# Kernel optimization log

Hardware: AMD Instinct MI355X
Metric: run time of the kernel (lower is better)

Reference implementation:

```python
import jax, jax.numpy as jnp
import numpy as np


def setup_inputs() -> dict:
    key = jax.random.key(0)
    k1, k2, k3 = jax.random.split(key, 3)
    B, S, D, H = 16, 4096, 512, 512
    inp = jax.random.normal(k1, (B, S, D), dtype=jnp.float32)
    # torch nn.Linear(D, 3*H): weight (3H, D), bias (3H,)
    W = jax.random.normal(k2, (3 * H, D), dtype=jnp.float32) * (1.0 / np.sqrt(D))
    b = jax.random.normal(k3, (3 * H,), dtype=jnp.float32) * 0.01
    return {"inp": inp, "W": W, "b": b}


def _forget_mult(z, f):
    # z, f: (B, S, H). h_t = f_t*z_t + (1-f_t)*h_{t-1}, h_{-1}=0 (hid=None)
    zt = jnp.swapaxes(z, 0, 1)  # (S, B, H)
    ft = jnp.swapaxes(f, 0, 1)
    h0 = jnp.zeros(z.shape[0:1] + z.shape[2:3], dtype=z.dtype)  # (B, H)

    def step(h, zf):
        zi, fi = zf
        h = fi * zi + (1.0 - fi) * h
        return h, h

    _, hs = jax.lax.scan(step, h0, (zt, ft))
    return jnp.swapaxes(hs, 0, 1)  # (B, S, H)


def reference(inp, W, b):
    # QRNNLayer forward: window=1, output_gate=True, batch_first=True,
    # backward=False, zoneout=0, hid=None.
    y = jnp.einsum('bsd,hd->bsh', inp, W) + b  # (B, S, 3H)
    z_gate, f_gate, o_gate = jnp.split(y, 3, axis=2)
    z_gate = jnp.tanh(z_gate)
    f_gate = jax.nn.sigmoid(f_gate)
    c_gate = _forget_mult(z_gate, f_gate)
    output = jax.nn.sigmoid(o_gate) * c_gate
    return output, c_gate[:, -1]
```

## Files before the change

kernel.cpp:

```cpp
#include <hip/hip_runtime.h>
#include <stdint.h>

#define Bdim 16
#define Sdim 4096
#define Hdim 512
#define Mdim (Bdim*Sdim)
#define N3   (3*Hdim)
#define Kdim 512
#define NCHUNK 64
#define CLEN  (Sdim/NCHUNK)

typedef __bf16 bf16;
typedef __bf16 bf16x4 __attribute__((ext_vector_type(4)));
typedef __bf16 bf16x8 __attribute__((ext_vector_type(8)));
typedef float  f32x4  __attribute__((ext_vector_type(4)));
typedef _Float16 f16;
typedef _Float16 f16x4 __attribute__((ext_vector_type(4)));
typedef _Float16 f16x8 __attribute__((ext_vector_type(8)));

__device__ __forceinline__ void gload_lds16(const void* g, void* l) {
  __builtin_amdgcn_global_load_lds(
      (const __attribute__((address_space(1))) uint32_t*)g,
      (__attribute__((address_space(3))) uint32_t*)l, 16, 0, 0);
}

__global__ void __launch_bounds__(256) cvt_kernel(const float4* __restrict__ in,
                                                  bf16x4* __restrict__ out, int n4) {
  int i = blockIdx.x * blockDim.x + threadIdx.x;
  if (i >= n4) return;
  float4 v = in[i];
  bf16x4 o;
  o.x = (bf16)v.x; o.y = (bf16)v.y; o.z = (bf16)v.z; o.w = (bf16)v.w;
  out[i] = o;
}

#define BM 256
#define BN 256
#define BK2 32
#define NT (Kdim/BK2)

__global__ void __launch_bounds__(512, 2) gemm_act_kernel(
    const bf16* __restrict__ A, const bf16* __restrict__ Wb,
    const float* __restrict__ bias,
    f16* __restrict__ zbuf, f16* __restrict__ fbuf, f16* __restrict__ ogbuf) {
  __shared__ char lds[65536];
  const int tid  = threadIdx.x;
  const int wid  = tid >> 6;
  const int lane = tid & 63;
  const int wr = wid >> 2, wc = wid & 3;
  const int bid = blockIdx.x;
  const int wg  = (bid & 7) * 192 + (bid >> 3);
  const int mt = wg / (N3 / BN);
  const int nt = wg % (N3 / BN);
  const int row0 = mt * BM;

  const bf16* Ag = A  + (size_t)row0 * Kdim;
  const bf16* Bg = Wb + (size_t)(nt * BN) * Kdim;

  uint32_t srcO[2];
  {
    int r_ = tid >> 2, slot = tid & 3;
    #pragma unroll
    for (int i = 0; i < 2; ++i) {
      int row = i * 128 + r_;
      srcO[i] = (uint32_t)(row * Kdim + ((slot ^ ((row >> 1) & 3)) << 3));
    }
  }
  const uint32_t dstBase = (uint32_t)(wid * 1024);

  uint32_t byteA[8], byteB[4];
  {
    int kslot = lane >> 4;
    #pragma unroll
    for (int m = 0; m < 8; ++m) {
      int row = wr * 128 + m * 16 + (lane & 15);
      byteA[m] = (uint32_t)(row * 64 + ((kslot ^ ((row >> 1) & 3)) << 4));
    }
    #pragma unroll
    for (int n = 0; n < 4; ++n) {
      int row = wc * 64 + n * 16 + (lane & 15);
      byteB[n] = (uint32_t)(16384 + row * 64 + ((kslot ^ ((row >> 1) & 3)) << 4));
    }
  }

  f32x4 acc[8][4];
  #pragma unroll
  for (int m = 0; m < 8; ++m)
    #pragma unroll
    for (int n = 0; n < 4; ++n)
      acc[m][n] = (f32x4){0.f, 0.f, 0.f, 0.f};

  {
    char* Ad = lds; char* Bd = lds + 16384;
    #pragma unroll
    for (int i = 0; i < 2; ++i) gload_lds16(Ag + srcO[i], Ad + i * 8192 + dstBase);
    #pragma unroll
    for (int i = 0; i < 2; ++i) gload_lds16(Bg + srcO[i], Bd + i * 8192 + dstBase);
  }
  __syncthreads();

  for (int t = 0; t < NT; ++t) {
    if (t + 1 < NT) {
      char* Ad = lds + ((t + 1) & 1) * 32768; char* Bd = Ad + 16384;
      #pragma unroll
      for (int i = 0; i < 2; ++i)
        gload_lds16(Ag + srcO[i] + (t + 1) * BK2, Ad + i * 8192 + dstBase);
      #pragma unroll
      for (int i = 0; i < 2; ++i)
        gload_lds16(Bg + srcO[i] + (t + 1) * BK2, Bd + i * 8192 + dstBase);
    }
    const char* Ab = lds + (t & 1) * 32768;
    bf16x8 af[8], bfrag[4];
    #pragma unroll
    for (int m = 0; m < 8; ++m) af[m] = *(const bf16x8*)(Ab + byteA[m]);
    #pragma unroll
    for (int n = 0; n < 4; ++n) bfrag[n] = *(const bf16x8*)(Ab + byteB[n]);
    __builtin_amdgcn_s_setprio(1);
    #pragma unroll
    for (int m = 0; m < 8; ++m)
      #pragma unroll
      for (int n = 0; n < 4; ++n)
        acc[m][n] = __builtin_amdgcn_mfma_f32_16x16x32_bf16(af[m], bfrag[n], acc[m][n], 0, 0, 0);
    __builtin_amdgcn_s_setprio(0);
    __syncthreads();
  }

  const int gate = nt >> 1;
  const int cbn  = (nt & 1) * 256;
  f16* dst = (gate == 0) ? zbuf : ((gate == 1) ? fbuf : ogbuf);
  float bv[4];
  #pragma unroll
  for (int n = 0; n < 4; ++n)
    bv[n] = bias[gate * Hdim + cbn + wc * 64 + n * 16 + (lane & 15)];

  #pragma unroll
  for (int R = 0; R < 2; ++R) {
    #pragma unroll
    for (int m4 = 0; m4 < 4; ++m4) {
      const int m = R * 4 + m4;
      #pragma unroll
      for (int n = 0; n < 4; ++n) {
        int col = wc * 64 + n * 16 + (lane & 15);
        #pragma unroll
        for (int r = 0; r < 4; ++r) {
          int Lrow = wr * 64 + m4 * 16 + (lane >> 4) * 4 + r;
          float y = acc[m][n][r] + bv[n];
          float v;
          if (gate == 0) {
            float e = __expf(2.f * y);
            v = 1.f - 2.f / (e + 1.f);
          } else {
            v = 1.f / (1.f + __expf(-y));
          }
          uint32_t byte = (uint32_t)(Lrow * 512 + col * 2) ^ ((uint32_t)(Lrow & 7) << 4);
          *(f16*)(lds + byte) = (f16)v;
        }
      }
    }
    __syncthreads();
    #pragma unroll
    for (int j = 0; j < 8; ++j) {
      int c = j * 512 + tid;
      int Lrow = c >> 5, col8 = c & 31;
      uint32_t byte = (uint32_t)(Lrow * 512 + col8 * 16) ^ ((uint32_t)(Lrow & 7) << 4);
      f16x8 v = *(const f16x8*)(lds + byte);
      int G = (Lrow >> 6) * 128 + R * 64 + (Lrow & 63);
      *(f16x8*)&dst[(size_t)(row0 + G) * Hdim + cbn + col8 * 8] = v;
    }
    __syncthreads();
  }
}

__global__ void __launch_bounds__(256) scanA_kernel(const f16x4* __restrict__ z4,
                                                    const f16x4* __restrict__ f4,
                                                    float* __restrict__ Pb,
                                                    float* __restrict__ Qb) {
  int u  = blockIdx.x * blockDim.x + threadIdx.x;
  int hq = u & 127;
  int bc = u >> 7;
  int b  = bc & (Bdim - 1);
  int c  = bc >> 4;
  size_t base = ((size_t)(b * Sdim + c * CLEN)) * 128 + hq;
  float P[4] = {1.f, 1.f, 1.f, 1.f}, Q[4] = {0.f, 0.f, 0.f, 0.f};
  #pragma unroll 4
  for (int s = 0; s < CLEN; ++s) {
    f16x4 fv = f4[base], zv = z4[base];
    #pragma unroll
    for (int j = 0; j < 4; ++j) {
      float f = (float)fv[j];
      Q[j] += f * ((float)zv[j] - Q[j]);
      P[j] *= (1.f - f);
    }
    base += 128;
  }
  int outi = ((c * Bdim + b) << 9) + hq * 4;
  *(float4*)&Pb[outi] = make_float4(P[0], P[1], P[2], P[3]);
  *(float4*)&Qb[outi] = make_float4(Q[0], Q[1], Q[2], Q[3]);
}

__global__ void __launch_bounds__(256) scanB_kernel(const float* __restrict__ Pb,
                                                    const float* __restrict__ Qb,
                                                    float* __restrict__ hin,
                                                    float* __restrict__ c_last) {
  int t = blockIdx.x * blockDim.x + threadIdx.x;
  int h = t & (Hdim - 1), b = t >> 9;
  float hs = 0.f;
  #pragma unroll 8
  for (int c = 0; c < NCHUNK; ++c) {
    hin[c * (Bdim * Hdim) + t] = hs;
    int u = ((c * Bdim + b) << 9) + h;
    hs = Pb[u] * hs + Qb[u];
  }
  c_last[t] = hs;
}

__global__ void __launch_bounds__(256) scanC_kernel(const f16x4* __restrict__ z4,
                                                    const f16x4* __restrict__ f4,
                                                    const f16x4* __restrict__ og4,
                                                    const float* __restrict__ hin,
                                                    float4* __restrict__ out4) {
  int u  = blockIdx.x * blockDim.x + threadIdx.x;
  int hq = u & 127;
  int bc = u >> 7;
  int b  = bc & (Bdim - 1);
  int c  = bc >> 4;
  float4 hv = *(const float4*)&hin[c * (Bdim * Hdim) + b * Hdim + hq * 4];
  float h[4] = {hv.x, hv.y, hv.z, hv.w};
  size_t base = ((size_t)(b * Sdim + c * CLEN)) * 128 + hq;
  #pragma unroll 4
  for (int s = 0; s < CLEN; ++s) {
    f16x4 fv = f4[base], zv = z4[base], ov = og4[base];
    float4 o;
    #pragma unroll
    for (int j = 0; j < 4; ++j) {
      h[j] += (float)fv[j] * ((float)zv[j] - h[j]);
    }
    o.x = (float)ov[0] * h[0]; o.y = (float)ov[1] * h[1];
    o.z = (float)ov[2] * h[2]; o.w = (float)ov[3] * h[3];
    out4[base] = o;
    base += 128;
  }
}

extern "C" void kernel_launch(void* const* d_in, const int* in_sizes, int n_in,
                              void* d_out, int out_size, void* d_ws, size_t ws_size,
                              hipStream_t stream) {
  const float* inp  = (const float*)d_in[0];
  const float* W    = (const float*)d_in[1];
  const float* bias = (const float*)d_in[2];
  float* out = (float*)d_out;

  char* ws = (char*)d_ws;
  bf16* Abf = (bf16*)(ws);
  bf16* Wbf = (bf16*)(ws + 67108864);
  f16*  zh  = (f16*) (ws + 68681728);
  f16*  fh  = (f16*) (ws + 135790592);
  f16*  ogh = (f16*) (ws + 202899456);
  float* Pb = (float*)(ws + 270008320);
  float* Qb = (float*)(ws + 272105472);
  float* hin= (float*)(ws + 274202624);

  {
    int n4 = (Mdim * Kdim) / 4;
    cvt_kernel<<<n4 / 256, 256, 0, stream>>>((const float4*)inp, (bf16x4*)Abf, n4);
  }
  {
    int n4 = (N3 * Kdim) / 4;
    cvt_kernel<<<n4 / 256, 256, 0, stream>>>((const float4*)W, (bf16x4*)Wbf, n4);
  }
  gemm_act_kernel<<<(Mdim / BM) * (N3 / BN), 512, 0, stream>>>(Abf, Wbf, bias,
                                                               zh, fh, ogh);
  scanA_kernel<<<(NCHUNK * Bdim * 128) / 256, 256, 0, stream>>>(
      (const f16x4*)zh, (const f16x4*)fh, Pb, Qb);
  scanB_kernel<<<(Bdim * Hdim) / 256, 256, 0, stream>>>(Pb, Qb, hin,
                                                        out + (size_t)Mdim * Hdim);
  scanC_kernel<<<(NCHUNK * Bdim * 128) / 256, 256, 0, stream>>>(
      (const f16x4*)zh, (const f16x4*)fh, (const f16x4*)ogh, hin, (float4*)out);
}
```

Baseline: 313.9 us.

## Shrink GEMM tile to 128 rows, fuse conversions, widen scan vectors, double chunks

The GEMM M-tile drops from 256 to 128 rows with smaller LDS buffers and launch bounds of 4 waves per SIMD. This aims at higher occupancy and more workgroups, at the cost of less A/B reuse per tile and the removal of the setprio hints. The two fp32→bf16 conversion launches are merged into one kernel. The scan kernels now process 8 halves per thread and the number of scan chunks doubles to 128, which gives more parallelism but adds more carry work in scanB.

```diff
diff --git a/kernel.cpp b/kernel.cpp
--- a/kernel.cpp
+++ b/kernel.cpp
@@ -7,7 +7,7 @@
 #define Mdim (Bdim*Sdim)
 #define N3   (3*Hdim)
 #define Kdim 512
-#define NCHUNK 64
+#define NCHUNK 128
 #define CLEN  (Sdim/NCHUNK)
 
 typedef __bf16 bf16;
@@ -15,7 +15,6 @@
 typedef __bf16 bf16x8 __attribute__((ext_vector_type(8)));
 typedef float  f32x4  __attribute__((ext_vector_type(4)));
 typedef _Float16 f16;
-typedef _Float16 f16x4 __attribute__((ext_vector_type(4)));
 typedef _Float16 f16x8 __attribute__((ext_vector_type(8)));
 
 __device__ __forceinline__ void gload_lds16(const void* g, void* l) {
@@ -24,32 +23,37 @@
       (__attribute__((address_space(3))) uint32_t*)l, 16, 0, 0);
 }
 
-__global__ void __launch_bounds__(256) cvt_kernel(const float4* __restrict__ in,
-                                                  bf16x4* __restrict__ out, int n4) {
+__global__ void __launch_bounds__(256) cvt2_kernel(const float4* __restrict__ a,
+                                                   bf16x4* __restrict__ oa, int nA,
+                                                   const float4* __restrict__ w,
+                                                   bf16x4* __restrict__ ow, int nW) {
   int i = blockIdx.x * blockDim.x + threadIdx.x;
-  if (i >= n4) return;
-  float4 v = in[i];
+  const float4* src; bf16x4* dst; int j;
+  if (i < nA) { src = a; dst = oa; j = i; }
+  else { j = i - nA; if (j >= nW) return; src = w; dst = ow; }
+  float4 v = src[j];
   bf16x4 o;
   o.x = (bf16)v.x; o.y = (bf16)v.y; o.z = (bf16)v.z; o.w = (bf16)v.w;
-  out[i] = o;
-}
-
-#define BM 256
+  dst[j] = o;
+}
+
+#define BM 128
 #define BN 256
 #define BK2 32
 #define NT (Kdim/BK2)
-
-__global__ void __launch_bounds__(512, 2) gemm_act_kernel(
+#define LBUF 24576
+
+__global__ void __launch_bounds__(512, 4) gemm_act_kernel(
     const bf16* __restrict__ A, const bf16* __restrict__ Wb,
     const float* __restrict__ bias,
     f16* __restrict__ zbuf, f16* __restrict__ fbuf, f16* __restrict__ ogbuf) {
-  __shared__ char lds[65536];
+  __shared__ char lds[2 * LBUF];
   const int tid  = threadIdx.x;
   const int wid  = tid >> 6;
   const int lane = tid & 63;
   const int wr = wid >> 2, wc = wid & 3;
   const int bid = blockIdx.x;
-  const int wg  = (bid & 7) * 192 + (bid >> 3);
+  const int wg  = (bid & 7) * 384 + (bid >> 3);
   const int mt = wg / (N3 / BN);
   const int nt = wg % (N3 / BN);
   const int row0 = mt * BM;
@@ -57,71 +61,69 @@
   const bf16* Ag = A  + (size_t)row0 * Kdim;
   const bf16* Bg = Wb + (size_t)(nt * BN) * Kdim;
 
-  uint32_t srcO[2];
-  {
-    int r_ = tid >> 2, slot = tid & 3;
-    #pragma unroll
-    for (int i = 0; i < 2; ++i) {
-      int row = i * 128 + r_;
-      srcO[i] = (uint32_t)(row * Kdim + ((slot ^ ((row >> 1) & 3)) << 3));
-    }
+  uint32_t srcA;
+  {
+    int row = tid >> 2, slot = tid & 3;
+    srcA = (uint32_t)(row * Kdim + ((slot ^ ((row >> 1) & 3)) << 3));
+  }
+  uint32_t srcB[2];
+  #pragma unroll
+  for (int i = 0; i < 2; ++i) {
+    int c = i * 512 + tid;
+    int row = c >> 2, slot = c & 3;
+    srcB[i] = (uint32_t)(row * Kdim + ((slot ^ ((row >> 1) & 3)) << 3));
   }
   const uint32_t dstBase = (uint32_t)(wid * 1024);
 
-  uint32_t byteA[8], byteB[4];
+  uint32_t byteA[4], byteB[4];
   {
     int kslot = lane >> 4;
     #pragma unroll
-    for (int m = 0; m < 8; ++m) {
-      int row = wr * 128 + m * 16 + (lane & 15);
+    for (int m = 0; m < 4; ++m) {
+      int row = wr * 64 + m * 16 + (lane & 15);
       byteA[m] = (uint32_t)(row * 64 + ((kslot ^ ((row >> 1) & 3)) << 4));
     }
     #pragma unroll
     for (int n = 0; n < 4; ++n) {
       int row = wc * 64 + n * 16 + (lane & 15);
-      byteB[n] = (uint32_t)(16384 + row * 64 + ((kslot ^ ((row >> 1) & 3)) << 4));
-    }
-  }
-
-  f32x4 acc[8][4];
-  #pragma unroll
-  for (int m = 0; m < 8; ++m)
+      byteB[n] = (uint32_t)(8192 + row * 64 + ((kslot ^ ((row >> 1) & 3)) << 4));
+    }
+  }
+
+  f32x4 acc[4][4];
+  #pragma unroll
+  for (int m = 0; m < 4; ++m)
     #pragma unroll
     for (int n = 0; n < 4; ++n)
       acc[m][n] = (f32x4){0.f, 0.f, 0.f, 0.f};
 
   {
-    char* Ad = lds; char* Bd = lds + 16384;
-    #pragma unroll
-    for (int i = 0; i < 2; ++i) gload_lds16(Ag + srcO[i], Ad + i * 8192 + dstBase);
-    #pragma unroll
-    for (int i = 0; i < 2; ++i) gload_lds16(Bg + srcO[i], Bd + i * 8192 + dstBase);
+    char* Ad = lds; char* Bd = lds + 8192;
+    gload_lds16(Ag + srcA, Ad + dstBase);
+    #pragma unroll
+    for (int i = 0; i < 2; ++i) gload_lds16(Bg + srcB[i], Bd + i * 8192 + dstBase);
   }
   __syncthreads();
 
   for (int t = 0; t < NT; ++t) {
     if (t + 1 < NT) {
-      char* Ad = lds + ((t + 1) & 1) * 32768; char* Bd = Ad + 16384;
+      char* Ad = lds + ((t + 1) & 1) * LBUF; char* Bd = Ad + 8192;
+      gload_lds16(Ag + srcA + (t + 1) * BK2, Ad + dstBase);
       #pragma unroll
       for (int i = 0; i < 2; ++i)
-        gload_lds16(Ag + srcO[i] + (t + 1) * BK2, Ad + i * 8192 + dstBase);
-      #pragma unroll
-      for (int i = 0; i < 2; ++i)
-        gload_lds16(Bg + srcO[i] + (t + 1) * BK2, Bd + i * 8192 + dstBase);
-    }
-    const char* Ab = lds + (t & 1) * 32768;
-    bf16x8 af[8], bfrag[4];
-    #pragma unroll
-    for (int m = 0; m < 8; ++m) af[m] = *(const bf16x8*)(Ab + byteA[m]);
+        gload_lds16(Bg + srcB[i] + (t + 1) * BK2, Bd + i * 8192 + dstBase);
+    }
+    const char* Ab = lds + (t & 1) * LBUF;
+    bf16x8 af[4], bfrag[4];
+    #pragma unroll
+    for (int m = 0; m < 4; ++m) af[m] = *(const bf16x8*)(Ab + byteA[m]);
     #pragma unroll
     for (int n = 0; n < 4; ++n) bfrag[n] = *(const bf16x8*)(Ab + byteB[n]);
-    __builtin_amdgcn_s_setprio(1);
-    #pragma unroll
-    for (int m = 0; m < 8; ++m)
+    #pragma unroll
+    for (int m = 0; m < 4; ++m)
       #pragma unroll
       for (int n = 0; n < 4; ++n)
         acc[m][n] = __builtin_amdgcn_mfma_f32_16x16x32_bf16(af[m], bfrag[n], acc[m][n], 0, 0, 0);
-    __builtin_amdgcn_s_setprio(0);
     __syncthreads();
   }
 
@@ -135,67 +137,71 @@
 
   #pragma unroll
   for (int R = 0; R < 2; ++R) {
-    #pragma unroll
-    for (int m4 = 0; m4 < 4; ++m4) {
-      const int m = R * 4 + m4;
+    if (wr == R) {
       #pragma unroll
-      for (int n = 0; n < 4; ++n) {
-        int col = wc * 64 + n * 16 + (lane & 15);
+      for (int m = 0; m < 4; ++m) {
         #pragma unroll
-        for (int r = 0; r < 4; ++r) {
-          int Lrow = wr * 64 + m4 * 16 + (lane >> 4) * 4 + r;
-          float y = acc[m][n][r] + bv[n];
-          float v;
-          if (gate == 0) {
-            float e = __expf(2.f * y);
-            v = 1.f - 2.f / (e + 1.f);
-          } else {
-            v = 1.f / (1.f + __expf(-y));
+        for (int n = 0; n < 4; ++n) {
+          int col = wc * 64 + n * 16 + (lane & 15);
+          #pragma unroll
+          for (int r = 0; r < 4; ++r) {
+            int Lrow = m * 16 + (lane >> 4) * 4 + r;
+            float y = acc[m][n][r] + bv[n];
+            float v;
+            if (gate == 0) {
+              float e = __expf(2.f * y);
+              v = 1.f - 2.f / (e + 1.f);
+            } else {
+              v = 1.f / (1.f + __expf(-y));
+            }
+            uint32_t byte = (uint32_t)(Lrow * 512 + col * 2) ^ ((uint32_t)(Lrow & 7) << 4);
+            *(f16*)(lds + byte) = (f16)v;
           }
-          uint32_t byte = (uint32_t)(Lrow * 512 + col * 2) ^ ((uint32_t)(Lrow & 7) << 4);
-          *(f16*)(lds + byte) = (f16)v;
         }
       }
     }
     __syncthreads();
     #pragma unroll
-    for (int j = 0; j < 8; ++j) {
+    for (int j = 0; j < 4; ++j) {
       int c = j * 512 + tid;
       int Lrow = c >> 5, col8 = c & 31;
       uint32_t byte = (uint32_t)(Lrow * 512 + col8 * 16) ^ ((uint32_t)(Lrow & 7) << 4);
       f16x8 v = *(const f16x8*)(lds + byte);
-      int G = (Lrow >> 6) * 128 + R * 64 + (Lrow & 63);
-      *(f16x8*)&dst[(size_t)(row0 + G) * Hdim + cbn + col8 * 8] = v;
+      *(f16x8*)&dst[(size_t)(row0 + R * 64 + Lrow) * Hdim + cbn + col8 * 8] = v;
     }
     __syncthreads();
   }
 }
 
-__global__ void __launch_bounds__(256) scanA_kernel(const f16x4* __restrict__ z4,
-                                                    const f16x4* __restrict__ f4,
+__global__ void __launch_bounds__(256) scanA_kernel(const f16x8* __restrict__ z8,
+                                                    const f16x8* __restrict__ f8,
                                                     float* __restrict__ Pb,
                                                     float* __restrict__ Qb) {
   int u  = blockIdx.x * blockDim.x + threadIdx.x;
-  int hq = u & 127;
-  int bc = u >> 7;
+  int ho = u & 63;
+  int bc = u >> 6;
   int b  = bc & (Bdim - 1);
   int c  = bc >> 4;
-  size_t base = ((size_t)(b * Sdim + c * CLEN)) * 128 + hq;
-  float P[4] = {1.f, 1.f, 1.f, 1.f}, Q[4] = {0.f, 0.f, 0.f, 0.f};
+  size_t base = ((size_t)(b * Sdim + c * CLEN)) * 64 + ho;
+  float P[8], Q[8];
+  #pragma unroll
+  for (int j = 0; j < 8; ++j) { P[j] = 1.f; Q[j] = 0.f; }
   #pragma unroll 4
   for (int s = 0; s < CLEN; ++s) {
-    f16x4 fv = f4[base], zv = z4[base];
-    #pragma unroll
-    for (int j = 0; j < 4; ++j) {
+    f16x8 fv = f8[base], zv = z8[base];
+    #pragma unroll
+    for (int j = 0; j < 8; ++j) {
       float f = (float)fv[j];
       Q[j] += f * ((float)zv[j] - Q[j]);
       P[j] *= (1.f - f);
     }
-    base += 128;
-  }
-  int outi = ((c * Bdim + b) << 9) + hq * 4;
-  *(float4*)&Pb[outi] = make_float4(P[0], P[1], P[2], P[3]);
-  *(float4*)&Qb[outi] = make_float4(Q[0], Q[1], Q[2], Q[3]);
+    base += 64;
+  }
+  int outi = ((c * Bdim + b) << 9) + ho * 8;
+  *(float4*)&Pb[outi]     = make_float4(P[0], P[1], P[2], P[3]);
+  *(float4*)&Pb[outi + 4] = make_float4(P[4], P[5], P[6], P[7]);
+  *(float4*)&Qb[outi]     = make_float4(Q[0], Q[1], Q[2], Q[3]);
+  *(float4*)&Qb[outi + 4] = make_float4(Q[4], Q[5], Q[6], Q[7]);
 }
 
 __global__ void __launch_bounds__(256) scanB_kernel(const float* __restrict__ Pb,
@@ -214,31 +220,35 @@
   c_last[t] = hs;
 }
 
-__global__ void __launch_bounds__(256) scanC_kernel(const f16x4* __restrict__ z4,
-                                                    const f16x4* __restrict__ f4,
-                                                    const f16x4* __restrict__ og4,
+__global__ void __launch_bounds__(256) scanC_kernel(const f16x8* __restrict__ z8,
+                                                    const f16x8* __restrict__ f8,
+                                                    const f16x8* __restrict__ og8,
                                                     const float* __restrict__ hin,
                                                     float4* __restrict__ out4) {
   int u  = blockIdx.x * blockDim.x + threadIdx.x;
-  int hq = u & 127;
-  int bc = u >> 7;
+  int ho = u & 63;
+  int bc = u >> 6;
   int b  = bc & (Bdim - 1);
   int c  = bc >> 4;
-  float4 hv = *(const float4*)&hin[c * (Bdim * Hdim) + b * Hdim + hq * 4];
-  float h[4] = {hv.x, hv.y, hv.z, hv.w};
-  size_t base = ((size_t)(b * Sdim + c * CLEN)) * 128 + hq;
+  const float* hp = &hin[c * (Bdim * Hdim) + b * Hdim + ho * 8];
+  float4 h0 = *(const float4*)hp;
+  float4 h1 = *(const float4*)(hp + 4);
+  float h[8] = {h0.x, h0.y, h0.z, h0.w, h1.x, h1.y, h1.z, h1.w};
+  size_t brow = (size_t)(b * Sdim + c * CLEN);
+  size_t base = brow * 64 + ho;
+  size_t obase = brow * 128 + ho * 2;
   #pragma unroll 4
   for (int s = 0; s < CLEN; ++s) {
-    f16x4 fv = f4[base], zv = z4[base], ov = og4[base];
-    float4 o;
-    #pragma unroll
-    for (int j = 0; j < 4; ++j) {
+    f16x8 fv = f8[base], zv = z8[base], ov = og8[base];
+    #pragma unroll
+    for (int j = 0; j < 8; ++j)
       h[j] += (float)fv[j] * ((float)zv[j] - h[j]);
-    }
-    o.x = (float)ov[0] * h[0]; o.y = (float)ov[1] * h[1];
-    o.z = (float)ov[2] * h[2]; o.w = (float)ov[3] * h[3];
-    out4[base] = o;
-    base += 128;
+    out4[obase]     = make_float4((float)ov[0] * h[0], (float)ov[1] * h[1],
+                                  (float)ov[2] * h[2], (float)ov[3] * h[3]);
+    out4[obase + 1] = make_float4((float)ov[4] * h[4], (float)ov[5] * h[5],
+                                  (float)ov[6] * h[6], (float)ov[7] * h[7]);
+    base += 64;
+    obase += 128;
   }
 }
 
@@ -257,23 +267,21 @@
   f16*  fh  = (f16*) (ws + 135790592);
   f16*  ogh = (f16*) (ws + 202899456);
   float* Pb = (float*)(ws + 270008320);
-  float* Qb = (float*)(ws + 272105472);
-  float* hin= (float*)(ws + 274202624);
-
-  {
-    int n4 = (Mdim * Kdim) / 4;
-    cvt_kernel<<<n4 / 256, 256, 0, stream>>>((const float4*)inp, (bf16x4*)Abf, n4);
-  }
-  {
-    int n4 = (N3 * Kdim) / 4;
-    cvt_kernel<<<n4 / 256, 256, 0, stream>>>((const float4*)W, (bf16x4*)Wbf, n4);
+  float* Qb = (float*)(ws + 274202624);
+  float* hin= (float*)(ws + 278396928);
+
+  {
+    int nA = (Mdim * Kdim) / 4;
+    int nW = (N3 * Kdim) / 4;
+    cvt2_kernel<<<(nA + nW + 255) / 256, 256, 0, stream>>>(
+        (const float4*)inp, (bf16x4*)Abf, nA, (const float4*)W, (bf16x4*)Wbf, nW);
   }
   gemm_act_kernel<<<(Mdim / BM) * (N3 / BN), 512, 0, stream>>>(Abf, Wbf, bias,
                                                                zh, fh, ogh);
-  scanA_kernel<<<(NCHUNK * Bdim * 128) / 256, 256, 0, stream>>>(
-      (const f16x4*)zh, (const f16x4*)fh, Pb, Qb);
+  scanA_kernel<<<(NCHUNK * Bdim * 64) / 256, 256, 0, stream>>>(
+      (const f16x8*)zh, (const f16x8*)fh, Pb, Qb);
   scanB_kernel<<<(Bdim * Hdim) / 256, 256, 0, stream>>>(Pb, Qb, hin,
                                                         out + (size_t)Mdim * Hdim);
-  scanC_kernel<<<(NCHUNK * Bdim * 128) / 256, 256, 0, stream>>>(
-      (const f16x4*)zh, (const f16x4*)fh, (const f16x4*)ogh, hin, (float4*)out);
-}
+  scanC_kernel<<<(NCHUNK * Bdim * 64) / 256, 256, 0, stream>>>(
+      (const f16x8*)zh, (const f16x8*)fh, (const f16x8*)ogh, hin, (float4*)out);
+}
```

New measurement: 299.8 us (median of 2 runs). 4.5% less time.
